# Optimization experiments

Measured on AMD Instinct MI355X. Metric: run time of the kernel, lower is better.

## Reference

```python
import jax, jax.numpy as jnp
import numpy as np

THRESHOLD = 0.1
N_HEAD = 16
NEG_INF = -1e9


def setup_inputs() -> dict:
    key = jax.random.key(0)
    ks = jax.random.split(key, 8)
    B, T, C = 2, 2048, 1024
    H, D, R = N_HEAD, C // N_HEAD, 8
    return {
        "x": jax.random.normal(ks[0], (B, T, C), dtype=jnp.float32),
        "W_attn": jax.random.normal(ks[1], (C, 3 * C), dtype=jnp.float32) * 0.02,
        "W_proj": jax.random.normal(ks[2], (C, C), dtype=jnp.float32) * 0.02,
        "W_recip": jax.random.normal(ks[3], (D, R), dtype=jnp.float32) * 0.02,
        "w_std": jax.random.uniform(ks[4], (H,), dtype=jnp.float32),
        "w_rec": jax.random.uniform(ks[5], (H,), dtype=jnp.float32),
        "w_disc": jax.random.uniform(ks[6], (H,), dtype=jnp.float32),
        "d_bias": jax.random.normal(ks[7], (H, T), dtype=jnp.float32) * 0.02,
    }


def reference(x, W_attn, W_proj, W_recip, w_std, w_rec, w_disc, d_bias):
    B, T, C = x.shape
    H = N_HEAD
    D = C // H
    R = W_recip.shape[1]
    D_std = D - R

    # QKV projection (Linear without bias)
    qkv = x @ W_attn  # [B,T,3C]
    q, k, v = jnp.split(qkv, 3, axis=2)

    def to_heads(t):
        return t.reshape(B, T, H, D).transpose(0, 2, 1, 3)  # [B,H,T,D]

    q, k, v = to_heads(q), to_heads(k), to_heads(v)

    # low-rank reciprocal projections
    QW = q @ W_recip  # [B,H,T,R]
    KW = k @ W_recip

    ws = jnp.sqrt(jnp.clip(w_std, 1e-8))[:, None, None]  # [H,1,1]
    wr = jnp.sqrt(jnp.clip(w_rec, 1e-8))[:, None, None]
    use_ra = (w_rec > THRESHOLD)[:, None, None]  # [H,1,1]

    # RA heads: augmented Q/K = [ws*Q_std | wr*KW] / [ws*K_std | wr*QW]
    q_aug = jnp.concatenate([ws * q[..., :D_std], wr * KW], axis=-1)
    k_aug = jnp.concatenate([ws * k[..., :D_std], wr * QW], axis=-1)
    q_eff = jnp.where(use_ra, q_aug, ws * q)
    k_eff = jnp.where(use_ra, k_aug, ws * k)

    # mean-centered discoverability column bias: [1,H,1,T]
    d = d_bias[:, :T]
    d = d - d.mean(axis=-1, keepdims=True)
    bias = (d * w_disc[:, None])[None, :, None, :]

    scale = 1.0 / jnp.sqrt(jnp.asarray(D, dtype=x.dtype))
    scores = jnp.einsum("bhid,bhjd->bhij", q_eff, k_eff) * scale + bias
    causal = jnp.tril(jnp.ones((T, T), dtype=bool))
    scores = jnp.where(causal[None, None], scores, NEG_INF)
    attn = jax.nn.softmax(scores, axis=-1)
    out = jnp.einsum("bhij,bhjd->bhid", attn, v)  # [B,H,T,D]

    out = out.transpose(0, 2, 1, 3).reshape(B, T, C)
    return out @ W_proj
```

## Files before the change

### kernel.cpp

```cpp
#include <hip/hip_runtime.h>
#include <hip/hip_bf16.h>

#define DEVI __device__ __forceinline__

typedef __attribute__((ext_vector_type(8))) short short8;
typedef __attribute__((ext_vector_type(4))) short short4v;
typedef __attribute__((ext_vector_type(4))) float floatx4;

static constexpr int B_ = 2, T_ = 2048, C_ = 1024, H_ = 16, D_ = 64;
static constexpr float LOG2E = 1.44269504088896f;

DEVI float bf2f(unsigned short u) {
    union { unsigned int i; float f; } v; v.i = ((unsigned int)u) << 16; return v.f;
}
DEVI unsigned short f2bf(float f) {
    union { float f; unsigned int i; } v; v.f = f;
    unsigned int x = v.i;
    return (unsigned short)((x + 0x7fffu + ((x >> 16) & 1u)) >> 16);
}
DEVI float fast_exp2(float x) {
#if __has_builtin(__builtin_amdgcn_exp2f)
    return __builtin_amdgcn_exp2f(x);
#else
    return __expf(x * 0.6931471805599453f);
#endif
}

DEVI void async16(const unsigned short* g, unsigned short* l) {
    __builtin_amdgcn_global_load_lds((const __attribute__((address_space(1))) void*)g,
                                     (__attribute__((address_space(3))) void*)l, 16, 0, 0);
}

__global__ __launch_bounds__(256) void k_cvt(const float* __restrict__ in,
                                             unsigned short* __restrict__ out, int n8) {
    int i = blockIdx.x * 256 + threadIdx.x;
    if (i >= n8) return;
    const float4* p = (const float4*)in + (size_t)i * 2;
    float4 a = p[0], b = p[1];
    union { unsigned short u[8]; short8 s; } r;
    r.u[0] = f2bf(a.x); r.u[1] = f2bf(a.y); r.u[2] = f2bf(a.z); r.u[3] = f2bf(a.w);
    r.u[4] = f2bf(b.x); r.u[5] = f2bf(b.y); r.u[6] = f2bf(b.z); r.u[7] = f2bf(b.w);
    *(short8*)&out[(size_t)i * 8] = r.s;
}

__global__ __launch_bounds__(256) void k_tr(const float* __restrict__ in,
                                            unsigned short* __restrict__ out, int K, int N) {
    __shared__ float tile[64][65];
    int k0 = blockIdx.y * 64, n0 = blockIdx.x * 64;
    int tid = threadIdx.x;
#pragma unroll
    for (int r = 0; r < 4; r++) {
        int ci = tid + r * 256;
        int row = ci >> 4, c4 = (ci & 15) * 4;
        float4 v = *(const float4*)&in[(size_t)(k0 + row) * N + n0 + c4];
        tile[row][c4 + 0] = v.x; tile[row][c4 + 1] = v.y;
        tile[row][c4 + 2] = v.z; tile[row][c4 + 3] = v.w;
    }
    __syncthreads();
#pragma unroll
    for (int r = 0; r < 2; r++) {
        int ci = tid + r * 256;
        int row = ci >> 3, c8 = (ci & 7) * 8;
        union { unsigned short u[8]; short8 s; } o;
#pragma unroll
        for (int j = 0; j < 8; j++) o.u[j] = f2bf(tile[c8 + j][row]);
        *(short8*)&out[(size_t)(n0 + row) * K + k0 + c8] = o.s;
    }
}

__global__ __launch_bounds__(256) void k_bias(const float* __restrict__ d_bias,
                                              const float* __restrict__ w_disc,
                                              float* __restrict__ bias) {
    int h = blockIdx.x, tid = threadIdx.x;
    __shared__ float red[256];
    float s = 0.f;
    for (int t = tid; t < T_; t += 256) s += d_bias[h * T_ + t];
    red[tid] = s;
    __syncthreads();
    for (int st = 128; st > 0; st >>= 1) {
        if (tid < st) red[tid] += red[tid + st];
        __syncthreads();
    }
    float mean = red[0] * (1.0f / T_);
    float wd = w_disc[h] * LOG2E;
    for (int t = tid; t < T_; t += 256) bias[h * T_ + t] = (d_bias[h * T_ + t] - mean) * wd;
}

template <typename OUT>
__global__ __launch_bounds__(256) void k_gemm(const unsigned short* __restrict__ A,
                                              const unsigned short* __restrict__ Bt,
                                              OUT* __restrict__ C, int M, int N, int K) {
    __shared__ __align__(16) unsigned short As[128 * 32];
    __shared__ __align__(16) unsigned short Bs[128 * 32];
    int m0 = blockIdx.y * 128, n0 = blockIdx.x * 128;
    int tid = threadIdx.x, l = tid & 63, w = tid >> 6;
    int wm = (w >> 1) * 64, wn = (w & 1) * 64;
    int lm = l & 15, lq = l >> 4;
    floatx4 acc[4][4];
#pragma unroll
    for (int a = 0; a < 4; a++)
#pragma unroll
        for (int b = 0; b < 4; b++) acc[a][b] = {0.f, 0.f, 0.f, 0.f};

    for (int k0 = 0; k0 < K; k0 += 32) {
        __syncthreads();
#pragma unroll
        for (int r = 0; r < 2; r++) {
            int ci = tid + r * 256;
            int row = ci >> 2, off = (ci & 3) * 8;
            async16(&A[(size_t)(m0 + row) * K + k0 + off], &As[row * 32 + off]);
            async16(&Bt[(size_t)(n0 + row) * K + k0 + off], &Bs[row * 32 + off]);
        }
        __syncthreads();
        short8 af[4], bf[4];
#pragma unroll
        for (int t = 0; t < 4; t++) af[t] = *(short8*)&As[(wm + t * 16 + lm) * 32 + lq * 8];
#pragma unroll
        for (int t = 0; t < 4; t++) bf[t] = *(short8*)&Bs[(wn + t * 16 + lm) * 32 + lq * 8];
#pragma unroll
        for (int tm = 0; tm < 4; tm++)
#pragma unroll
            for (int tn = 0; tn < 4; tn++)
                acc[tm][tn] = __builtin_amdgcn_mfma_f32_16x16x32_bf16(af[tm], bf[tn], acc[tm][tn], 0, 0, 0);
    }
#pragma unroll
    for (int tm = 0; tm < 4; tm++)
#pragma unroll
        for (int tn = 0; tn < 4; tn++) {
            int row = m0 + wm + tm * 16 + lq * 4;
            int col = n0 + wn + tn * 16 + lm;
#pragma unroll
            for (int r = 0; r < 4; r++) {
                float v = acc[tm][tn][r];
                if constexpr (sizeof(OUT) == 2) C[(size_t)(row + r) * N + col] = (OUT)f2bf(v);
                else                            C[(size_t)(row + r) * N + col] = v;
            }
        }
}

__global__ __launch_bounds__(256) void k_build(const unsigned short* __restrict__ qkv,
                                               const float* __restrict__ W_recip,
                                               const float* __restrict__ w_std,
                                               const float* __restrict__ w_rec,
                                               unsigned short* __restrict__ qe,
                                               unsigned short* __restrict__ ke) {
    __shared__ float Wr[64 * 8];
    int tid = threadIdx.x;
    for (int i = tid; i < 512; i += 256) Wr[i] = W_recip[i];
    __syncthreads();
    int g = blockIdx.x * 256 + tid;
    int t = g & (T_ - 1), h = (g >> 11) & (H_ - 1), b = g >> 15;
    float ws = sqrtf(fmaxf(w_std[h], 1e-8f));
    float wr = sqrtf(fmaxf(w_rec[h], 1e-8f));
    bool ra = w_rec[h] > 0.1f;
    const unsigned short* qrow = qkv + (size_t)(b * T_ + t) * 3072 + h * 64;
    const unsigned short* krow = qrow + 1024;
    float q[64], k[64];
#pragma unroll
    for (int i = 0; i < 8; i++) {
        short8 qv = *(const short8*)&qrow[i * 8];
        short8 kv = *(const short8*)&krow[i * 8];
#pragma unroll
        for (int j = 0; j < 8; j++) {
            q[i * 8 + j] = bf2f((unsigned short)qv[j]);
            k[i * 8 + j] = bf2f((unsigned short)kv[j]);
        }
    }
    float QW[8], KW[8];
#pragma unroll
    for (int r = 0; r < 8; r++) { QW[r] = 0.f; KW[r] = 0.f; }
#pragma unroll
    for (int d = 0; d < 64; d++)
#pragma unroll
        for (int r = 0; r < 8; r++) {
            QW[r] += q[d] * Wr[d * 8 + r];
            KW[r] += k[d] * Wr[d * 8 + r];
        }
    const float qscale = 0.125f * LOG2E;
    size_t tbase = (size_t)(b * H_ + h) * 131072 + (size_t)(t >> 4) * 1024 + (size_t)(t & 15) * 8;
#pragma unroll
    for (int i = 0; i < 8; i++) {
        union { unsigned short u[8]; short8 s; } uq, uk;
#pragma unroll
        for (int j = 0; j < 8; j++) {
            int d = i * 8 + j;
            float qv, kv;
            if (ra && d >= 56) { qv = wr * KW[d - 56]; kv = wr * QW[d - 56]; }
            else               { qv = ws * q[d];       kv = ws * k[d]; }
            uq.u[j] = f2bf(qv * qscale);
            uk.u[j] = f2bf(kv);
        }
        size_t off = tbase + (size_t)(i >> 2) * 512 + (size_t)(i & 3) * 128;
        *(short8*)&qe[off] = uq.s;
        *(short8*)&ke[off] = uk.s;
    }
}

__global__ __launch_bounds__(256) void k_vtr(const unsigned short* __restrict__ qkv,
                                             unsigned short* __restrict__ vt) {
    int tid = threadIdx.x;
    int g = blockIdx.x;
    int tchunk = g & 63;
    int h = (g >> 6) & 15, b = g >> 10;
    int d = tid & 63, tg = tid >> 6;
    int t0 = tchunk * 32 + tg * 8;
    union { unsigned short u[8]; short8 s; } v;
#pragma unroll
    for (int i = 0; i < 8; i++)
        v.u[i] = qkv[(size_t)(b * T_ + t0 + i) * 3072 + 2048 + h * 64 + d];
    size_t off = (size_t)((b * H_ + h)) * 131072 + (size_t)tchunk * 2048 +
                 (size_t)(d >> 4) * 512 + (size_t)tg * 128 + (size_t)(d & 15) * 8;
    *(short8*)&vt[off] = v.s;
}

DEVI void online_softmax(float sv[4][4], float& m_i, float& l_i, floatx4* O,
                         unsigned int pk[4][2]) {
    float mx = sv[0][0];
#pragma unroll
    for (int js = 0; js < 4; js++)
#pragma unroll
        for (int r = 0; r < 4; r++) mx = fmaxf(mx, sv[js][r]);
    mx = fmaxf(mx, __shfl_xor(mx, 16));
    mx = fmaxf(mx, __shfl_xor(mx, 32));
    float mn = fmaxf(m_i, mx);
    float alpha = fast_exp2(m_i - mn);
    m_i = mn;
    float rs = 0.f;
#pragma unroll
    for (int js = 0; js < 4; js++)
#pragma unroll
        for (int r = 0; r < 4; r++) {
            float p = fast_exp2(sv[js][r] - mn);
            sv[js][r] = p;
            rs += p;
        }
    rs += __shfl_xor(rs, 16);
    rs += __shfl_xor(rs, 32);
    l_i = l_i * alpha + rs;
#pragma unroll
    for (int dt = 0; dt < 4; dt++) {
        floatx4 o = O[dt];
        o[0] *= alpha; o[1] *= alpha; o[2] *= alpha; o[3] *= alpha;
        O[dt] = o;
    }
#pragma unroll
    for (int js = 0; js < 4; js++) {
        pk[js][0] = (unsigned int)f2bf(sv[js][0]) | ((unsigned int)f2bf(sv[js][1]) << 16);
        pk[js][1] = (unsigned int)f2bf(sv[js][2]) | ((unsigned int)f2bf(sv[js][3]) << 16);
    }
}

DEVI short8 make_pf(const unsigned int pk[4][2], int c, int srcLo, int srcHi, bool hi) {
    int a0 = __shfl((int)pk[2 * c][0], srcLo);
    int a1 = __shfl((int)pk[2 * c][1], srcLo);
    int a2 = __shfl((int)pk[2 * c][0], srcHi);
    int a3 = __shfl((int)pk[2 * c][1], srcHi);
    int b0 = __shfl((int)pk[2 * c + 1][0], srcLo);
    int b1 = __shfl((int)pk[2 * c + 1][1], srcLo);
    int b2 = __shfl((int)pk[2 * c + 1][0], srcHi);
    int b3 = __shfl((int)pk[2 * c + 1][1], srcHi);
    union { int i[4]; short8 s; } pf;
    pf.i[0] = hi ? b0 : a0;
    pf.i[1] = hi ? b1 : a1;
    pf.i[2] = hi ? b2 : a2;
    pf.i[3] = hi ? b3 : a3;
    return pf.s;
}

__global__ __launch_bounds__(256) void k_attn(const unsigned short* __restrict__ qe,
                                              const unsigned short* __restrict__ ke,
                                              const unsigned short* __restrict__ vt,
                                              const float* __restrict__ bias,
                                              unsigned short* __restrict__ obf) {
    int bh = blockIdx.y;
    int b = bh >> 4, h = bh & 15;
    int tid = threadIdx.x, l = tid & 63, w = tid >> 6;
    int lm = l & 15, lq = l >> 4;
    int l8 = l * 8;
    const size_t hb = (size_t)bh * 131072;
    const unsigned short* qeh = qe + hb;
    const unsigned short* keh = ke + hb;
    const unsigned short* vth = vt + hb;
    const float* biash = bias + h * T_;

    int gA = blockIdx.x * 4 + w;
    int gB = 127 - gA;
    int itA = (gA >> 2) + 1, itB = (gB >> 2) + 1;
    int irowA = gA * 16 + lm, irowB = gB * 16 + lm;

    short8 qA0 = *(const short8*)(qeh + (size_t)gA * 1024 + l8);
    short8 qA1 = *(const short8*)(qeh + (size_t)gA * 1024 + 512 + l8);
    short8 qB0 = *(const short8*)(qeh + (size_t)gB * 1024 + l8);
    short8 qB1 = *(const short8*)(qeh + (size_t)gB * 1024 + 512 + l8);

    floatx4 OA[4], OB[4];
#pragma unroll
    for (int i = 0; i < 4; i++) { OA[i] = {0.f, 0.f, 0.f, 0.f}; OB[i] = {0.f, 0.f, 0.f, 0.f}; }
    float mA = -3e38f, lA = 0.f, mB = -3e38f, lB = 0.f;

    const int srcLo = ((lq & 1) * 2) * 16 + lm;
    const int srcHi = srcLo + 16;
    const bool hi = (lq >> 1) & 1;

    int j0 = 0;
    for (int s = 0; s < itA; s++, j0 += 64) {
        float svA[4][4], svB[4][4];
#pragma unroll
        for (int js = 0; js < 4; js++) {
            const unsigned short* kp = keh + (size_t)((j0 >> 4) + js) * 1024 + l8;
            short8 kf0 = *(const short8*)kp;
            short8 kf1 = *(const short8*)(kp + 512);
            floatx4 sa = {0.f, 0.f, 0.f, 0.f}, sb = {0.f, 0.f, 0.f, 0.f};
            sa = __builtin_amdgcn_mfma_f32_16x16x32_bf16(kf0, qA0, sa, 0, 0, 0);
            sa = __builtin_amdgcn_mfma_f32_16x16x32_bf16(kf1, qA1, sa, 0, 0, 0);
            sb = __builtin_amdgcn_mfma_f32_16x16x32_bf16(kf0, qB0, sb, 0, 0, 0);
            sb = __builtin_amdgcn_mfma_f32_16x16x32_bf16(kf1, qB1, sb, 0, 0, 0);
            int jb = j0 + js * 16 + lq * 4;
            float4 bj = *(const float4*)&biash[jb];
            float bv[4] = {bj.x, bj.y, bj.z, bj.w};
#pragma unroll
            for (int r = 0; r < 4; r++) {
                svA[js][r] = (jb + r <= irowA) ? (sa[r] + bv[r]) : -1e9f;
                svB[js][r] = sb[r] + bv[r];
            }
        }
        unsigned int pkA[4][2], pkB[4][2];
        online_softmax(svA, mA, lA, OA, pkA);
        online_softmax(svB, mB, lB, OB, pkB);
#pragma unroll
        for (int c = 0; c < 2; c++) {
            short8 pfA = make_pf(pkA, c, srcLo, srcHi, hi);
            short8 pfB = make_pf(pkB, c, srcLo, srcHi, hi);
#pragma unroll
            for (int dt = 0; dt < 4; dt++) {
                short8 vf = *(const short8*)(vth + (size_t)((j0 >> 5) + c) * 2048 + dt * 512 + l8);
                OA[dt] = __builtin_amdgcn_mfma_f32_16x16x32_bf16(vf, pfA, OA[dt], 0, 0, 0);
                OB[dt] = __builtin_amdgcn_mfma_f32_16x16x32_bf16(vf, pfB, OB[dt], 0, 0, 0);
            }
        }
    }
    for (int s = itA; s < itB; s++, j0 += 64) {
        float svB[4][4];
#pragma unroll
        for (int js = 0; js < 4; js++) {
            const unsigned short* kp = keh + (size_t)((j0 >> 4) + js) * 1024 + l8;
            short8 kf0 = *(const short8*)kp;
            short8 kf1 = *(const short8*)(kp + 512);
            floatx4 sb = {0.f, 0.f, 0.f, 0.f};
            sb = __builtin_amdgcn_mfma_f32_16x16x32_bf16(kf0, qB0, sb, 0, 0, 0);
            sb = __builtin_amdgcn_mfma_f32_16x16x32_bf16(kf1, qB1, sb, 0, 0, 0);
            int jb = j0 + js * 16 + lq * 4;
            float4 bj = *(const float4*)&biash[jb];
            float bv[4] = {bj.x, bj.y, bj.z, bj.w};
#pragma unroll
            for (int r = 0; r < 4; r++)
                svB[js][r] = (jb + r <= irowB) ? (sb[r] + bv[r]) : -1e9f;
        }
        unsigned int pkB[4][2];
        online_softmax(svB, mB, lB, OB, pkB);
#pragma unroll
        for (int c = 0; c < 2; c++) {
            short8 pfB = make_pf(pkB, c, srcLo, srcHi, hi);
#pragma unroll
            for (int dt = 0; dt < 4; dt++) {
                short8 vf = *(const short8*)(vth + (size_t)((j0 >> 5) + c) * 2048 + dt * 512 + l8);
                OB[dt] = __builtin_amdgcn_mfma_f32_16x16x32_bf16(vf, pfB, OB[dt], 0, 0, 0);
            }
        }
    }
    {
        float inv = 1.0f / lA;
        unsigned short* orow = obf + (size_t)(b * T_ + irowA) * C_ + h * 64;
#pragma unroll
        for (int dt = 0; dt < 4; dt++) {
            union { unsigned short u[4]; short4v s; } o;
#pragma unroll
            for (int r = 0; r < 4; r++) o.u[r] = f2bf(OA[dt][r] * inv);
            *(short4v*)&orow[dt * 16 + lq * 4] = o.s;
        }
    }
    {
        float inv = 1.0f / lB;
        unsigned short* orow = obf + (size_t)(b * T_ + irowB) * C_ + h * 64;
#pragma unroll
        for (int dt = 0; dt < 4; dt++) {
            union { unsigned short u[4]; short4v s; } o;
#pragma unroll
            for (int r = 0; r < 4; r++) o.u[r] = f2bf(OB[dt][r] * inv);
            *(short4v*)&orow[dt * 16 + lq * 4] = o.s;
        }
    }
}

extern "C" void kernel_launch(void* const* d_in, const int* in_sizes, int n_in,
                              void* d_out, int out_size, void* d_ws, size_t ws_size,
                              hipStream_t stream) {
    const float* x       = (const float*)d_in[0];
    const float* W_attn  = (const float*)d_in[1];
    const float* W_proj  = (const float*)d_in[2];
    const float* W_recip = (const float*)d_in[3];
    const float* w_std   = (const float*)d_in[4];
    const float* w_rec   = (const float*)d_in[5];
    const float* w_disc  = (const float*)d_in[6];
    const float* d_bias  = (const float*)d_in[7];

    char* ws = (char*)d_ws;
    size_t o = 0;
    unsigned short* x_bf = (unsigned short*)(ws + o); o += (size_t)4096 * 1024 * 2;
    unsigned short* wa_t = (unsigned short*)(ws + o); o += (size_t)3072 * 1024 * 2;
    unsigned short* wp_t = (unsigned short*)(ws + o); o += (size_t)1024 * 1024 * 2;
    unsigned short* qkv  = (unsigned short*)(ws + o); o += (size_t)4096 * 3072 * 2;
    unsigned short* qe   = (unsigned short*)(ws + o); o += (size_t)32 * 2048 * 64 * 2;
    unsigned short* ke   = (unsigned short*)(ws + o); o += (size_t)32 * 2048 * 64 * 2;
    unsigned short* vt   = (unsigned short*)(ws + o); o += (size_t)32 * 2048 * 64 * 2;
    unsigned short* obf  = (unsigned short*)(ws + o); o += (size_t)4096 * 1024 * 2;
    float* bias          = (float*)(ws + o);          o += (size_t)16 * 2048 * 4;

    k_cvt<<<2048, 256, 0, stream>>>(x, x_bf, 524288);
    k_tr<<<dim3(48, 16), 256, 0, stream>>>(W_attn, wa_t, 1024, 3072);
    k_tr<<<dim3(16, 16), 256, 0, stream>>>(W_proj, wp_t, 1024, 1024);
    k_bias<<<16, 256, 0, stream>>>(d_bias, w_disc, bias);
    k_gemm<unsigned short><<<dim3(24, 32), 256, 0, stream>>>(x_bf, wa_t, qkv, 4096, 3072, 1024);
    k_build<<<256, 256, 0, stream>>>(qkv, W_recip, w_std, w_rec, qe, ke);
    k_vtr<<<2048, 256, 0, stream>>>(qkv, vt);
    k_attn<<<dim3(16, 32), 256, 0, stream>>>(qe, ke, vt, bias, obf);
    k_gemm<float><<<dim3(8, 32), 256, 0, stream>>>(obf, wp_t, (float*)d_out, 4096, 1024, 1024);
}
```

Baseline: 229.7 us.

## Merge prep kernels, software-pipeline attention loads, and retile output projection

Folds the conversion, weight transposes and bias prep into one launch, and merges the q/k build with the V transpose, to cut launch overhead. The attention loop is restructured into a single loop that prefetches the next K fragments and loads V up front. Causal masking now runs only on the diagonal tile, the bf16 packing uses a hardware pack instruction, and occupancy is hinted through launch bounds. The output projection gets a 128x64 tile GEMM, doubling the block count to fill more CUs. The extra live registers may limit the occupancy the launch bound asks for.

```diff
diff --git a/kernel.cpp b/kernel.cpp
--- a/kernel.cpp
+++ b/kernel.cpp
@@ -17,6 +17,16 @@
     union { float f; unsigned int i; } v; v.f = f;
     unsigned int x = v.i;
     return (unsigned short)((x + 0x7fffu + ((x >> 16) & 1u)) >> 16);
+}
+DEVI unsigned int pk2bf(float lo, float hi) {
+#if __has_builtin(__builtin_amdgcn_cvt_pk_bf16_f32)
+    typedef __attribute__((ext_vector_type(2))) __bf16 bf16x2;
+    union { bf16x2 v; unsigned int u; } r;
+    r.v = __builtin_amdgcn_cvt_pk_bf16_f32(lo, hi);
+    return r.u;
+#else
+    return (unsigned int)f2bf(lo) | ((unsigned int)f2bf(hi) << 16);
+#endif
 }
 DEVI float fast_exp2(float x) {
 #if __has_builtin(__builtin_amdgcn_exp2f)
@@ -31,23 +41,9 @@
                                      (__attribute__((address_space(3))) void*)l, 16, 0, 0);
 }
 
-__global__ __launch_bounds__(256) void k_cvt(const float* __restrict__ in,
-                                             unsigned short* __restrict__ out, int n8) {
-    int i = blockIdx.x * 256 + threadIdx.x;
-    if (i >= n8) return;
-    const float4* p = (const float4*)in + (size_t)i * 2;
-    float4 a = p[0], b = p[1];
-    union { unsigned short u[8]; short8 s; } r;
-    r.u[0] = f2bf(a.x); r.u[1] = f2bf(a.y); r.u[2] = f2bf(a.z); r.u[3] = f2bf(a.w);
-    r.u[4] = f2bf(b.x); r.u[5] = f2bf(b.y); r.u[6] = f2bf(b.z); r.u[7] = f2bf(b.w);
-    *(short8*)&out[(size_t)i * 8] = r.s;
-}
-
-__global__ __launch_bounds__(256) void k_tr(const float* __restrict__ in,
-                                            unsigned short* __restrict__ out, int K, int N) {
-    __shared__ float tile[64][65];
-    int k0 = blockIdx.y * 64, n0 = blockIdx.x * 64;
-    int tid = threadIdx.x;
+DEVI void tr_body(const float* in, unsigned short* out, int K, int N, int bx, int by,
+                  int tid, float (*tile)[65]) {
+    int k0 = by * 64, n0 = bx * 64;
 #pragma unroll
     for (int r = 0; r < 4; r++) {
         int ci = tid + r * 256;
@@ -68,22 +64,46 @@
     }
 }
 
-__global__ __launch_bounds__(256) void k_bias(const float* __restrict__ d_bias,
+__global__ __launch_bounds__(256) void k_prep(const float* __restrict__ x,
+                                              const float* __restrict__ W_attn,
+                                              const float* __restrict__ W_proj,
+                                              const float* __restrict__ d_bias,
                                               const float* __restrict__ w_disc,
+                                              unsigned short* __restrict__ x_bf,
+                                              unsigned short* __restrict__ wa_t,
+                                              unsigned short* __restrict__ wp_t,
                                               float* __restrict__ bias) {
-    int h = blockIdx.x, tid = threadIdx.x;
+    __shared__ float tile[64][65];
     __shared__ float red[256];
-    float s = 0.f;
-    for (int t = tid; t < T_; t += 256) s += d_bias[h * T_ + t];
-    red[tid] = s;
-    __syncthreads();
-    for (int st = 128; st > 0; st >>= 1) {
-        if (tid < st) red[tid] += red[tid + st];
+    int bid = blockIdx.x, tid = threadIdx.x;
+    if (bid < 2048) {
+        int i = bid * 256 + tid;
+        const float4* p = (const float4*)x + (size_t)i * 2;
+        float4 a = p[0], b = p[1];
+        union { unsigned short u[8]; short8 s; } r;
+        r.u[0] = f2bf(a.x); r.u[1] = f2bf(a.y); r.u[2] = f2bf(a.z); r.u[3] = f2bf(a.w);
+        r.u[4] = f2bf(b.x); r.u[5] = f2bf(b.y); r.u[6] = f2bf(b.z); r.u[7] = f2bf(b.w);
+        *(short8*)&x_bf[(size_t)i * 8] = r.s;
+    } else if (bid < 2816) {
+        int idx = bid - 2048;
+        tr_body(W_attn, wa_t, 1024, 3072, idx % 48, idx / 48, tid, tile);
+    } else if (bid < 3072) {
+        int idx = bid - 2816;
+        tr_body(W_proj, wp_t, 1024, 1024, idx & 15, idx >> 4, tid, tile);
+    } else {
+        int h = bid - 3072;
+        float s = 0.f;
+        for (int t = tid; t < T_; t += 256) s += d_bias[h * T_ + t];
+        red[tid] = s;
         __syncthreads();
-    }
-    float mean = red[0] * (1.0f / T_);
-    float wd = w_disc[h] * LOG2E;
-    for (int t = tid; t < T_; t += 256) bias[h * T_ + t] = (d_bias[h * T_ + t] - mean) * wd;
+        for (int st = 128; st > 0; st >>= 1) {
+            if (tid < st) red[tid] += red[tid + st];
+            __syncthreads();
+        }
+        float mean = red[0] * (1.0f / T_);
+        float wd = w_disc[h] * LOG2E;
+        for (int t = tid; t < T_; t += 256) bias[h * T_ + t] = (d_bias[h * T_ + t] - mean) * wd;
+    }
 }
 
 template <typename OUT>
@@ -138,17 +158,58 @@
         }
 }
 
-__global__ __launch_bounds__(256) void k_build(const unsigned short* __restrict__ qkv,
-                                               const float* __restrict__ W_recip,
-                                               const float* __restrict__ w_std,
-                                               const float* __restrict__ w_rec,
-                                               unsigned short* __restrict__ qe,
-                                               unsigned short* __restrict__ ke) {
-    __shared__ float Wr[64 * 8];
-    int tid = threadIdx.x;
-    for (int i = tid; i < 512; i += 256) Wr[i] = W_recip[i];
-    __syncthreads();
-    int g = blockIdx.x * 256 + tid;
+__global__ __launch_bounds__(256) void k_gemm64(const unsigned short* __restrict__ A,
+                                                const unsigned short* __restrict__ Bt,
+                                                float* __restrict__ C, int M, int N, int K) {
+    __shared__ __align__(16) unsigned short As[128 * 32];
+    __shared__ __align__(16) unsigned short Bs[64 * 32];
+    int m0 = blockIdx.y * 128, n0 = blockIdx.x * 64;
+    int tid = threadIdx.x, l = tid & 63, w = tid >> 6;
+    int wm = w * 32;
+    int lm = l & 15, lq = l >> 4;
+    floatx4 acc[2][4];
+#pragma unroll
+    for (int a = 0; a < 2; a++)
+#pragma unroll
+        for (int b = 0; b < 4; b++) acc[a][b] = {0.f, 0.f, 0.f, 0.f};
+
+    for (int k0 = 0; k0 < K; k0 += 32) {
+        __syncthreads();
+#pragma unroll
+        for (int r = 0; r < 2; r++) {
+            int ci = tid + r * 256;
+            int row = ci >> 2, off = (ci & 3) * 8;
+            async16(&A[(size_t)(m0 + row) * K + k0 + off], &As[row * 32 + off]);
+        }
+        {
+            int row = tid >> 2, off = (tid & 3) * 8;
+            async16(&Bt[(size_t)(n0 + row) * K + k0 + off], &Bs[row * 32 + off]);
+        }
+        __syncthreads();
+        short8 af[2], bf[4];
+#pragma unroll
+        for (int t = 0; t < 2; t++) af[t] = *(short8*)&As[(wm + t * 16 + lm) * 32 + lq * 8];
+#pragma unroll
+        for (int t = 0; t < 4; t++) bf[t] = *(short8*)&Bs[(t * 16 + lm) * 32 + lq * 8];
+#pragma unroll
+        for (int tm = 0; tm < 2; tm++)
+#pragma unroll
+            for (int tn = 0; tn < 4; tn++)
+                acc[tm][tn] = __builtin_amdgcn_mfma_f32_16x16x32_bf16(af[tm], bf[tn], acc[tm][tn], 0, 0, 0);
+    }
+#pragma unroll
+    for (int tm = 0; tm < 2; tm++)
+#pragma unroll
+        for (int tn = 0; tn < 4; tn++) {
+            int row = m0 + wm + tm * 16 + lq * 4;
+            int col = n0 + tn * 16 + lm;
+#pragma unroll
+            for (int r = 0; r < 4; r++) C[(size_t)(row + r) * N + col] = acc[tm][tn][r];
+        }
+}
+
+DEVI void build_body(const unsigned short* qkv, const float* Wr, const float* w_std,
+                     const float* w_rec, unsigned short* qe, unsigned short* ke, int g) {
     int t = g & (T_ - 1), h = (g >> 11) & (H_ - 1), b = g >> 15;
     float ws = sqrtf(fmaxf(w_std[h], 1e-8f));
     float wr = sqrtf(fmaxf(w_rec[h], 1e-8f));
@@ -196,21 +257,33 @@
     }
 }
 
-__global__ __launch_bounds__(256) void k_vtr(const unsigned short* __restrict__ qkv,
-                                             unsigned short* __restrict__ vt) {
-    int tid = threadIdx.x;
-    int g = blockIdx.x;
-    int tchunk = g & 63;
-    int h = (g >> 6) & 15, b = g >> 10;
-    int d = tid & 63, tg = tid >> 6;
-    int t0 = tchunk * 32 + tg * 8;
-    union { unsigned short u[8]; short8 s; } v;
-#pragma unroll
-    for (int i = 0; i < 8; i++)
-        v.u[i] = qkv[(size_t)(b * T_ + t0 + i) * 3072 + 2048 + h * 64 + d];
-    size_t off = (size_t)((b * H_ + h)) * 131072 + (size_t)tchunk * 2048 +
-                 (size_t)(d >> 4) * 512 + (size_t)tg * 128 + (size_t)(d & 15) * 8;
-    *(short8*)&vt[off] = v.s;
+__global__ __launch_bounds__(256) void k_bv(const unsigned short* __restrict__ qkv,
+                                            const float* __restrict__ W_recip,
+                                            const float* __restrict__ w_std,
+                                            const float* __restrict__ w_rec,
+                                            unsigned short* __restrict__ qe,
+                                            unsigned short* __restrict__ ke,
+                                            unsigned short* __restrict__ vt) {
+    __shared__ float Wr[64 * 8];
+    int bid = blockIdx.x, tid = threadIdx.x;
+    if (bid < 256) {
+        for (int i = tid; i < 512; i += 256) Wr[i] = W_recip[i];
+        __syncthreads();
+        build_body(qkv, Wr, w_std, w_rec, qe, ke, bid * 256 + tid);
+    } else {
+        int g = bid - 256;
+        int tchunk = g & 63;
+        int h = (g >> 6) & 15, b = g >> 10;
+        int d = tid & 63, tg = tid >> 6;
+        int t0 = tchunk * 32 + tg * 8;
+        union { unsigned short u[8]; short8 s; } v;
+#pragma unroll
+        for (int i = 0; i < 8; i++)
+            v.u[i] = qkv[(size_t)(b * T_ + t0 + i) * 3072 + 2048 + h * 64 + d];
+        size_t off = (size_t)((b * H_ + h)) * 131072 + (size_t)tchunk * 2048 +
+                     (size_t)(d >> 4) * 512 + (size_t)tg * 128 + (size_t)(d & 15) * 8;
+        *(short8*)&vt[off] = v.s;
+    }
 }
 
 DEVI void online_softmax(float sv[4][4], float& m_i, float& l_i, floatx4* O,
@@ -245,8 +318,8 @@
     }
 #pragma unroll
     for (int js = 0; js < 4; js++) {
-        pk[js][0] = (unsigned int)f2bf(sv[js][0]) | ((unsigned int)f2bf(sv[js][1]) << 16);
-        pk[js][1] = (unsigned int)f2bf(sv[js][2]) | ((unsigned int)f2bf(sv[js][3]) << 16);
+        pk[js][0] = pk2bf(sv[js][0], sv[js][1]);
+        pk[js][1] = pk2bf(sv[js][2], sv[js][3]);
     }
 }
 
@@ -267,11 +340,13 @@
     return pf.s;
 }
 
-__global__ __launch_bounds__(256) void k_attn(const unsigned short* __restrict__ qe,
-                                              const unsigned short* __restrict__ ke,
-                                              const unsigned short* __restrict__ vt,
-                                              const float* __restrict__ bias,
-                                              unsigned short* __restrict__ obf) {
+struct KF { short8 lo[4]; short8 hi[4]; };
+
+__global__ __launch_bounds__(256, 2) void k_attn(const unsigned short* __restrict__ qe,
+                                                 const unsigned short* __restrict__ ke,
+                                                 const unsigned short* __restrict__ vt,
+                                                 const float* __restrict__ bias,
+                                                 unsigned short* __restrict__ obf) {
     int bh = blockIdx.y;
     int b = bh >> 4, h = bh & 15;
     int tid = threadIdx.x, l = tid & 63, w = tid >> 6;
@@ -302,81 +377,127 @@
     const int srcHi = srcLo + 16;
     const bool hi = (lq >> 1) & 1;
 
-    int j0 = 0;
-    for (int s = 0; s < itA; s++, j0 += 64) {
-        float svA[4][4], svB[4][4];
+    KF kfa, kfb;
+#pragma unroll
+    for (int js = 0; js < 4; js++) {
+        const unsigned short* kp = keh + (size_t)js * 1024 + l8;
+        kfa.lo[js] = *(const short8*)kp;
+        kfa.hi[js] = *(const short8*)(kp + 512);
+    }
+
+    auto step = [&](int s, KF& cur, KF& nxt) {
+        int j0 = s * 64;
+        bool doA = (s < itA);
+        bool maskA = (s == itA - 1);
+        bool maskB = (s == itB - 1);
+        {
+            const unsigned short* kb = keh + (size_t)(s + 1) * 4096 + l8;
+#pragma unroll
+            for (int js = 0; js < 4; js++) {
+                nxt.lo[js] = *(const short8*)(kb + js * 1024);
+                nxt.hi[js] = *(const short8*)(kb + js * 1024 + 512);
+            }
+        }
+        short8 vfr[2][4];
+#pragma unroll
+        for (int c = 0; c < 2; c++)
+#pragma unroll
+            for (int dt = 0; dt < 4; dt++)
+                vfr[c][dt] = *(const short8*)(vth + (size_t)((j0 >> 5) + c) * 2048 + dt * 512 + l8);
+        floatx4 sb4[4], sa4[4];
 #pragma unroll
         for (int js = 0; js < 4; js++) {
-            const unsigned short* kp = keh + (size_t)((j0 >> 4) + js) * 1024 + l8;
-            short8 kf0 = *(const short8*)kp;
-            short8 kf1 = *(const short8*)(kp + 512);
-            floatx4 sa = {0.f, 0.f, 0.f, 0.f}, sb = {0.f, 0.f, 0.f, 0.f};
-            sa = __builtin_amdgcn_mfma_f32_16x16x32_bf16(kf0, qA0, sa, 0, 0, 0);
-            sa = __builtin_amdgcn_mfma_f32_16x16x32_bf16(kf1, qA1, sa, 0, 0, 0);
-            sb = __builtin_amdgcn_mfma_f32_16x16x32_bf16(kf0, qB0, sb, 0, 0, 0);
-            sb = __builtin_amdgcn_mfma_f32_16x16x32_bf16(kf1, qB1, sb, 0, 0, 0);
-            int jb = j0 + js * 16 + lq * 4;
-            float4 bj = *(const float4*)&biash[jb];
-            float bv[4] = {bj.x, bj.y, bj.z, bj.w};
-#pragma unroll
-            for (int r = 0; r < 4; r++) {
-                svA[js][r] = (jb + r <= irowA) ? (sa[r] + bv[r]) : -1e9f;
-                svB[js][r] = sb[r] + bv[r];
-            }
-        }
-        unsigned int pkA[4][2], pkB[4][2];
-        online_softmax(svA, mA, lA, OA, pkA);
-        online_softmax(svB, mB, lB, OB, pkB);
-#pragma unroll
-        for (int c = 0; c < 2; c++) {
-            short8 pfA = make_pf(pkA, c, srcLo, srcHi, hi);
-            short8 pfB = make_pf(pkB, c, srcLo, srcHi, hi);
-#pragma unroll
-            for (int dt = 0; dt < 4; dt++) {
-                short8 vf = *(const short8*)(vth + (size_t)((j0 >> 5) + c) * 2048 + dt * 512 + l8);
-                OA[dt] = __builtin_amdgcn_mfma_f32_16x16x32_bf16(vf, pfA, OA[dt], 0, 0, 0);
-                OB[dt] = __builtin_amdgcn_mfma_f32_16x16x32_bf16(vf, pfB, OB[dt], 0, 0, 0);
-            }
-        }
-    }
-    for (int s = itA; s < itB; s++, j0 += 64) {
+            floatx4 sb = {0.f, 0.f, 0.f, 0.f};
+            sb = __builtin_amdgcn_mfma_f32_16x16x32_bf16(cur.lo[js], qB0, sb, 0, 0, 0);
+            sb = __builtin_amdgcn_mfma_f32_16x16x32_bf16(cur.hi[js], qB1, sb, 0, 0, 0);
+            sb4[js] = sb;
+        }
+        if (doA) {
+#pragma unroll
+            for (int js = 0; js < 4; js++) {
+                floatx4 sa = {0.f, 0.f, 0.f, 0.f};
+                sa = __builtin_amdgcn_mfma_f32_16x16x32_bf16(cur.lo[js], qA0, sa, 0, 0, 0);
+                sa = __builtin_amdgcn_mfma_f32_16x16x32_bf16(cur.hi[js], qA1, sa, 0, 0, 0);
+                sa4[js] = sa;
+            }
+        }
+        float bv[4][4];
+#pragma unroll
+        for (int js = 0; js < 4; js++) {
+            float4 bj = *(const float4*)&biash[j0 + js * 16 + lq * 4];
+            bv[js][0] = bj.x; bv[js][1] = bj.y; bv[js][2] = bj.z; bv[js][3] = bj.w;
+        }
         float svB[4][4];
 #pragma unroll
-        for (int js = 0; js < 4; js++) {
-            const unsigned short* kp = keh + (size_t)((j0 >> 4) + js) * 1024 + l8;
-            short8 kf0 = *(const short8*)kp;
-            short8 kf1 = *(const short8*)(kp + 512);
-            floatx4 sb = {0.f, 0.f, 0.f, 0.f};
-            sb = __builtin_amdgcn_mfma_f32_16x16x32_bf16(kf0, qB0, sb, 0, 0, 0);
-            sb = __builtin_amdgcn_mfma_f32_16x16x32_bf16(kf1, qB1, sb, 0, 0, 0);
-            int jb = j0 + js * 16 + lq * 4;
-            float4 bj = *(const float4*)&biash[jb];
-            float bv[4] = {bj.x, bj.y, bj.z, bj.w};
-#pragma unroll
-            for (int r = 0; r < 4; r++)
-                svB[js][r] = (jb + r <= irowB) ? (sb[r] + bv[r]) : -1e9f;
+        for (int js = 0; js < 4; js++)
+#pragma unroll
+            for (int r = 0; r < 4; r++) svB[js][r] = sb4[js][r] + bv[js][r];
+        if (maskB) {
+#pragma unroll
+            for (int js = 0; js < 4; js++) {
+                int jb = j0 + js * 16 + lq * 4;
+#pragma unroll
+                for (int r = 0; r < 4; r++)
+                    if (jb + r > irowB) svB[js][r] = -1e9f;
+            }
         }
         unsigned int pkB[4][2];
         online_softmax(svB, mB, lB, OB, pkB);
-#pragma unroll
-        for (int c = 0; c < 2; c++) {
-            short8 pfB = make_pf(pkB, c, srcLo, srcHi, hi);
-#pragma unroll
-            for (int dt = 0; dt < 4; dt++) {
-                short8 vf = *(const short8*)(vth + (size_t)((j0 >> 5) + c) * 2048 + dt * 512 + l8);
-                OB[dt] = __builtin_amdgcn_mfma_f32_16x16x32_bf16(vf, pfB, OB[dt], 0, 0, 0);
-            }
-        }
-    }
+
+        if (doA) {
+            float svA[4][4];
+#pragma unroll
+            for (int js = 0; js < 4; js++)
+#pragma unroll
+                for (int r = 0; r < 4; r++) svA[js][r] = sa4[js][r] + bv[js][r];
+            if (maskA) {
+#pragma unroll
+                for (int js = 0; js < 4; js++) {
+                    int jb = j0 + js * 16 + lq * 4;
+#pragma unroll
+                    for (int r = 0; r < 4; r++)
+                        if (jb + r > irowA) svA[js][r] = -1e9f;
+                }
+            }
+            unsigned int pkA[4][2];
+            online_softmax(svA, mA, lA, OA, pkA);
+#pragma unroll
+            for (int c = 0; c < 2; c++) {
+                short8 pfA = make_pf(pkA, c, srcLo, srcHi, hi);
+                short8 pfB = make_pf(pkB, c, srcLo, srcHi, hi);
+#pragma unroll
+                for (int dt = 0; dt < 4; dt++) {
+                    OA[dt] = __builtin_amdgcn_mfma_f32_16x16x32_bf16(vfr[c][dt], pfA, OA[dt], 0, 0, 0);
+                    OB[dt] = __builtin_amdgcn_mfma_f32_16x16x32_bf16(vfr[c][dt], pfB, OB[dt], 0, 0, 0);
+                }
+            }
+        } else {
+#pragma unroll
+            for (int c = 0; c < 2; c++) {
+                short8 pfB = make_pf(pkB, c, srcLo, srcHi, hi);
+#pragma unroll
+                for (int dt = 0; dt < 4; dt++)
+                    OB[dt] = __builtin_amdgcn_mfma_f32_16x16x32_bf16(vfr[c][dt], pfB, OB[dt], 0, 0, 0);
+            }
+        }
+    };
+
+    int s = 0;
+    for (; s + 2 <= itB; s += 2) {
+        step(s, kfa, kfb);
+        step(s + 1, kfb, kfa);
+    }
+    if (s < itB) step(s, kfa, kfb);
+
     {
         float inv = 1.0f / lA;
         unsigned short* orow = obf + (size_t)(b * T_ + irowA) * C_ + h * 64;
 #pragma unroll
         for (int dt = 0; dt < 4; dt++) {
-            union { unsigned short u[4]; short4v s; } o;
+            union { unsigned short u[4]; short4v s4; } o;
 #pragma unroll
             for (int r = 0; r < 4; r++) o.u[r] = f2bf(OA[dt][r] * inv);
-            *(short4v*)&orow[dt * 16 + lq * 4] = o.s;
+            *(short4v*)&orow[dt * 16 + lq * 4] = o.s4;
         }
     }
     {
@@ -384,10 +505,10 @@
         unsigned short* orow = obf + (size_t)(b * T_ + irowB) * C_ + h * 64;
 #pragma unroll
         for (int dt = 0; dt < 4; dt++) {
-            union { unsigned short u[4]; short4v s; } o;
+            union { unsigned short u[4]; short4v s4; } o;
 #pragma unroll
             for (int r = 0; r < 4; r++) o.u[r] = f2bf(OB[dt][r] * inv);
-            *(short4v*)&orow[dt * 16 + lq * 4] = o.s;
+            *(short4v*)&orow[dt * 16 + lq * 4] = o.s4;
         }
     }
 }
@@ -416,13 +537,9 @@
     unsigned short* obf  = (unsigned short*)(ws + o); o += (size_t)4096 * 1024 * 2;
     float* bias          = (float*)(ws + o);          o += (size_t)16 * 2048 * 4;
 
-    k_cvt<<<2048, 256, 0, stream>>>(x, x_bf, 524288);
-    k_tr<<<dim3(48, 16), 256, 0, stream>>>(W_attn, wa_t, 1024, 3072);
-    k_tr<<<dim3(16, 16), 256, 0, stream>>>(W_proj, wp_t, 1024, 1024);
-    k_bias<<<16, 256, 0, stream>>>(d_bias, w_disc, bias);
+    k_prep<<<3088, 256, 0, stream>>>(x, W_attn, W_proj, d_bias, w_disc, x_bf, wa_t, wp_t, bias);
     k_gemm<unsigned short><<<dim3(24, 32), 256, 0, stream>>>(x_bf, wa_t, qkv, 4096, 3072, 1024);
-    k_build<<<256, 256, 0, stream>>>(qkv, W_recip, w_std, w_rec, qe, ke);
-    k_vtr<<<2048, 256, 0, stream>>>(qkv, vt);
+    k_bv<<<2304, 256, 0, stream>>>(qkv, W_recip, w_std, w_rec, qe, ke, vt);
     k_attn<<<dim3(16, 32), 256, 0, stream>>>(qe, ke, vt, bias, obf);
-    k_gemm<float><<<dim3(8, 32), 256, 0, stream>>>(obf, wp_t, (float*)d_out, 4096, 1024, 1024);
-}
+    k_gemm64<<<dim3(16, 32), 256, 0, stream>>>(obf, wp_t, (float*)d_out, 4096, 1024, 1024);
+}
```

After: 209.7 us. 8.7% less time.
